# Kernel optimization log

Measured on AMD Instinct MI355X. Metric: run time of the kernel, lower is better.

Reference implementation:

```python
import jax, jax.numpy as jnp
import numpy as np

B, IN_UNIT, C, U, OUT = 256, 8, 1152, 10, 16  # batch, input_unit, input_channels, num_unit, unit_size
NUM_ROUTES = 4


def squash(s, axis):
    # norm_sqr/(1+norm_sqr) * s/||s||, matching the torch squash (no eps, as in source)
    n2 = jnp.sum(s * s, axis=axis, keepdims=True)
    return n2 / (1.0 + n2) * (s / jnp.sqrt(n2))


def setup_inputs() -> dict:
    key = jax.random.key(0)
    k1, k2 = jax.random.split(key)
    x = jax.random.normal(k1, (B, IN_UNIT, C), dtype=jnp.float32)
    W = jax.random.normal(k2, (C, U, OUT, IN_UNIT), dtype=jnp.float32)  # torch weights squeezed of leading 1
    return {"x": x, "W": W}


def reference(x, W):
    # x: [B, in_unit, C] -> [B, C, in_unit]
    xt = jnp.transpose(x, (0, 2, 1))
    # predict_vectors u_hat[b,c,u,:] = W[c,u] @ x[b,c]  -> [B, C, U, OUT]
    u_hat = jnp.einsum('bci,cuoi->bcuo', xt, W)
    b = jnp.zeros((C, U), dtype=x.dtype)  # routing logits (torch: [1,C,U,1] zeros)
    v = None
    for _ in range(NUM_ROUTES):
        c = jax.nn.softmax(b, axis=1)                      # softmax over num_unit (dim=2 in torch layout)
        s = jnp.einsum('cu,bcuo->buo', c, u_hat)           # weighted sum over input capsules -> [B,U,OUT]
        v = squash(s, axis=2)                              # squash over unit_size dim
        agreement = jnp.einsum('bcuo,buo->bcu', u_hat, v)  # u_hat^T v, -> [B,C,U]
        b = b + jnp.mean(agreement, axis=0)                # mean over batch, as in source
    return v[..., None]  # [B, U, OUT, 1] matching vec_out.squeeze(1)
```

## Files before the change

kernel.cpp:

```cpp
#include <hip/hip_runtime.h>
#include <cstdint>
#include <cstddef>

typedef _Float16 half_t;
typedef __attribute__((ext_vector_type(8))) _Float16 f16x8;
typedef __attribute__((ext_vector_type(4))) _Float16 f16x4;
typedef __attribute__((ext_vector_type(4))) float f32x4;
typedef unsigned int uint_t;

#define OFF_WH   0
#define OFF_XHF  2949120
#define OFF_XKH  7667712
#define OFF_VHF  12386304
#define OFF_AG   12468224
#define WS_NEED  12606464

__device__ __forceinline__ void gload16(const void* g, void* l) {
  __builtin_amdgcn_global_load_lds(
      (const __attribute__((address_space(1))) unsigned int*)g,
      (__attribute__((address_space(3))) unsigned int*)l, 16, 0, 0);
}

__global__ void k_setup(const float* __restrict__ x, const float* __restrict__ W,
                        half_t* __restrict__ wh, half_t* __restrict__ xhf,
                        half_t* __restrict__ xkh) {
  int bid = blockIdx.x, tid = threadIdx.x;
  if (bid < 720) {
    int gid = bid * 256 + tid;
    const float4 a0 = *(const float4*)(W + (size_t)gid * 8);
    const float4 a1 = *(const float4*)(W + (size_t)gid * 8 + 4);
    f16x8 o;
    o[0] = (half_t)a0.x; o[1] = (half_t)a0.y; o[2] = (half_t)a0.z; o[3] = (half_t)a0.w;
    o[4] = (half_t)a1.x; o[5] = (half_t)a1.y; o[6] = (half_t)a1.z; o[7] = (half_t)a1.w;
    *(f16x8*)(wh + (size_t)gid * 8) = o;
  } else if (bid < 976) {
    int b = bid - 720;
    __shared__ float lds_f[9216];
    const float4* xr = (const float4*)(x + (size_t)b * 9216);
    for (int t = tid; t < 2304; t += 256) {
      float4 v = xr[t];
      lds_f[t * 4 + 0] = v.x; lds_f[t * 4 + 1] = v.y;
      lds_f[t * 4 + 2] = v.z; lds_f[t * 4 + 3] = v.w;
    }
    __syncthreads();
    for (int t = tid; t < 1152; t += 256) {
      f16x8 o;
#pragma unroll
      for (int i = 0; i < 8; ++i) o[i] = (half_t)lds_f[i * 1152 + t];
      *(f16x8*)(xhf + (size_t)b * 9216 + t * 8) = o;
    }
  } else {
    int tb = bid - 976;
    int kt = tb % 288, bt = tb / 288;
    int c0 = kt * 4, b0 = bt * 32;
    __shared__ float lt[32][36];
    int bl = tid >> 3, ch = tid & 7;
    float4 v = *(const float4*)(x + (size_t)(b0 + bl) * 9216 + ch * 1152 + c0);
    lt[bl][0 * 8 + ch] = v.x;
    lt[bl][1 * 8 + ch] = v.y;
    lt[bl][2 * 8 + ch] = v.z;
    lt[bl][3 * 8 + ch] = v.w;
    __syncthreads();
    int kl = tid >> 3, bg = tid & 7;
    f16x4 h;
    h[0] = (half_t)lt[bg * 4 + 0][kl];
    h[1] = (half_t)lt[bg * 4 + 1][kl];
    h[2] = (half_t)lt[bg * 4 + 2][kl];
    h[3] = (half_t)lt[bg * 4 + 3][kl];
    *(f16x4*)(xkh + (size_t)(kt * 32 + kl) * 256 + b0 + bg * 4) = h;
  }
}

__global__ __launch_bounds__(1024) void k_g1sq(const half_t* __restrict__ xhf,
                                               const half_t* __restrict__ wh,
                                               const float* __restrict__ ag,
                                               half_t* __restrict__ vhfT,
                                               float* __restrict__ out, int it) {
  int mb = blockIdx.x, nt = blockIdx.y;
  int tid = threadIdx.x;
  int wv = tid >> 6, l = tid & 63, lm = l & 15, lgp = l >> 4;
  __shared__ __align__(16) half_t cwf[1152];
  __shared__ __align__(16) half_t stage[16][3][2][512];
  __shared__ __align__(16) float red[16][64][4];

  for (int c = tid; c < 1152; c += 1024) {
    float lv[10] = {0.f, 0.f, 0.f, 0.f, 0.f, 0.f, 0.f, 0.f, 0.f, 0.f};
    for (int t = 0; t < it; ++t)
#pragma unroll
      for (int u = 0; u < 10; ++u) lv[u] += ag[(size_t)(t * 10 + u) * 1152 + c];
    float mx = lv[0];
#pragma unroll
    for (int u = 1; u < 10; ++u) mx = fmaxf(mx, lv[u]);
    float ssum = 0.f, sel = 0.f;
#pragma unroll
    for (int u = 0; u < 10; ++u) {
      float e = __expf((lv[u] - mx) * (1.0f / 256.0f));
      ssum += e;
      if (u == nt) sel = e;
    }
    cwf[c] = (half_t)(sel / ssum);
  }
  __syncthreads();

  const half_t* xbase = xhf + (size_t)(mb * 16 + (l >> 2)) * 9216 + (l & 3) * 8;
  const half_t* wbase = wh + ((size_t)(lgp * 10 + nt) * 16 + lm) * 8;
  int kt0 = wv * 18;
  int cbase = kt0 * 4 + lgp;
#define ISSUE(J)                                                                   \
  do {                                                                             \
    int kt_ = kt0 + (J);                                                           \
    gload16(xbase + (size_t)kt_ * 32, &stage[wv][(J) % 3][0][0]);                  \
    gload16(wbase + (size_t)kt_ * 5120, &stage[wv][(J) % 3][1][0]);                \
  } while (0)

  ISSUE(0);
  ISSUE(1);
  ISSUE(2);

  f32x4 acc0 = {0.f, 0.f, 0.f, 0.f};
  f32x4 acc1 = {0.f, 0.f, 0.f, 0.f};
#pragma unroll
  for (int j = 0; j < 18; ++j) {
    const int buf = j % 3;
    if (j <= 15) {
      asm volatile("s_waitcnt vmcnt(4)" ::: "memory");
    } else if (j == 16) {
      asm volatile("s_waitcnt vmcnt(2)" ::: "memory");
    } else {
      asm volatile("s_waitcnt vmcnt(0)" ::: "memory");
    }
    __builtin_amdgcn_sched_barrier(0);
    f16x8 af = *(const f16x8*)&stage[wv][buf][0][lm * 32 + lgp * 8];
    f16x8 wf = *(const f16x8*)&stage[wv][buf][1][l * 8];
    half_t sc = cwf[cbase + j * 4];
    f16x8 bsc = wf * sc;
    if ((j & 1) == 0) acc0 = __builtin_amdgcn_mfma_f32_16x16x32_f16(af, bsc, acc0, 0, 0, 0);
    else              acc1 = __builtin_amdgcn_mfma_f32_16x16x32_f16(af, bsc, acc1, 0, 0, 0);
    __builtin_amdgcn_sched_barrier(0);
    if (j + 3 < 18) ISSUE(j + 3);
    __builtin_amdgcn_sched_barrier(0);
  }
#undef ISSUE
  acc0[0] += acc1[0]; acc0[1] += acc1[1]; acc0[2] += acc1[2]; acc0[3] += acc1[3];
  *(f32x4*)&red[wv][l][0] = acc0;
  __syncthreads();
  if (wv == 0) {
    float4 s = make_float4(0.f, 0.f, 0.f, 0.f);
#pragma unroll
    for (int w = 0; w < 16; ++w) {
      s.x += red[w][l][0]; s.y += red[w][l][1];
      s.z += red[w][l][2]; s.w += red[w][l][3];
    }
    float4 n2 = make_float4(s.x * s.x, s.y * s.y, s.z * s.z, s.w * s.w);
#pragma unroll
    for (int off = 1; off < 16; off <<= 1) {
      n2.x += __shfl_xor(n2.x, off);
      n2.y += __shfl_xor(n2.y, off);
      n2.z += __shfl_xor(n2.z, off);
      n2.w += __shfl_xor(n2.w, off);
    }
    float4 vv;
    vv.x = s.x * (n2.x / ((1.f + n2.x) * sqrtf(n2.x)));
    vv.y = s.y * (n2.y / ((1.f + n2.y) * sqrtf(n2.y)));
    vv.z = s.z * (n2.z / ((1.f + n2.z) * sqrtf(n2.z)));
    vv.w = s.w * (n2.w / ((1.f + n2.w) * sqrtf(n2.w)));
    if (it == 3) {
      float* ob = out + (size_t)(mb * 16 + lgp * 4) * 160 + nt * 16 + lm;
      ob[0 * 160] = vv.x; ob[1 * 160] = vv.y; ob[2 * 160] = vv.z; ob[3 * 160] = vv.w;
    } else {
      f16x4 h;
      h[0] = (half_t)vv.x; h[1] = (half_t)vv.y; h[2] = (half_t)vv.z; h[3] = (half_t)vv.w;
      *(f16x4*)(vhfT + (size_t)(nt * 16 + lm) * 256 + mb * 16 + lgp * 4) = h;
    }
  }
}

__global__ __launch_bounds__(256) void k_g2(const half_t* __restrict__ xkh,
                                            const half_t* __restrict__ vhfT,
                                            const float* __restrict__ W,
                                            float* __restrict__ ag, int it) {
  int cb = blockIdx.x;
  int tid = threadIdx.x;
  int wv = tid >> 6, l = tid & 63, lm = l & 15, lgp = l >> 4;
  int mt = cb * 4 + wv;
  f32x4 z = {0.f, 0.f, 0.f, 0.f};
  f32x4 acc[10];
#pragma unroll
  for (int nt = 0; nt < 10; ++nt) acc[nt] = z;

#pragma unroll
  for (int bt = 0; bt < 8; ++bt) {
    f16x8 af = *(const f16x8*)(xkh + (size_t)(mt * 16 + lm) * 256 + bt * 32 + lgp * 8);
#pragma unroll
    for (int nt = 0; nt < 10; ++nt) {
      f16x8 bfr = *(const f16x8*)(vhfT + (size_t)(nt * 16 + lm) * 256 + bt * 32 + lgp * 8);
      acc[nt] = __builtin_amdgcn_mfma_f32_16x16x32_f16(af, bfr, acc[nt], 0, 0, 0);
    }
  }
  int cc = mt * 2 + (lgp >> 1);
  int i0 = (lgp & 1) * 4;
  float* agt = ag + (size_t)it * 11520;
#pragma unroll
  for (int nt = 0; nt < 10; ++nt) {
    float4 wdv = *(const float4*)(W + ((size_t)(cc * 10 + nt) * 16 + lm) * 8 + i0);
    float q = acc[nt][0] * wdv.x + acc[nt][1] * wdv.y
            + acc[nt][2] * wdv.z + acc[nt][3] * wdv.w;
    q += __shfl_xor(q, 1);
    q += __shfl_xor(q, 2);
    q += __shfl_xor(q, 4);
    q += __shfl_xor(q, 8);
    q += __shfl_xor(q, 16);
    if (lm == 0 && (lgp & 1) == 0)
      agt[(size_t)nt * 1152 + cc] = q;
  }
}

extern "C" void kernel_launch(void* const* d_in, const int* in_sizes, int n_in,
                              void* d_out, int out_size, void* d_ws, size_t ws_size,
                              hipStream_t stream) {
  const float* x = (const float*)d_in[0];
  const float* W = (const float*)d_in[1];
  float* out = (float*)d_out;
  char* ws = (char*)d_ws;
  if (ws_size < WS_NEED) return;

  half_t* wh  = (half_t*)(ws + OFF_WH);
  half_t* xhf = (half_t*)(ws + OFF_XHF);
  half_t* xkh = (half_t*)(ws + OFF_XKH);
  half_t* vhfT= (half_t*)(ws + OFF_VHF);
  float*  ag  = (float*)(ws + OFF_AG);

  k_setup<<<dim3(3280), dim3(256), 0, stream>>>(x, W, wh, xhf, xkh);
  for (int it = 0; it < 4; ++it) {
    k_g1sq<<<dim3(16, 10), dim3(1024), 0, stream>>>(xhf, wh, ag, vhfT, out, it);
    if (it < 3)
      k_g2<<<dim3(144), dim3(256), 0, stream>>>(xkh, vhfT, W, ag, it);
  }
}
```

Baseline: 121.3 us.

## Fuse routing softmax into agreement kernel and deepen g1 load pipeline

The softmax over routing logits moves out of every k_g1sq block and into k_g2. k_g2 now accumulates the logits in place and writes fp16 coupling weights once per channel, so each of the 160 g1 blocks no longer re-reads all past agreement slices and recomputes the exponentials. The first iteration uses a constant 0.1 weight. The g1 LDS staging ring also grows from 3 to 4 buffers with matching waitcnt thresholds, for more loads in flight, at the cost of extra shared memory per block.

```diff
diff --git a/kernel.cpp b/kernel.cpp
--- a/kernel.cpp
+++ b/kernel.cpp
@@ -12,8 +12,9 @@
 #define OFF_XHF  2949120
 #define OFF_XKH  7667712
 #define OFF_VHF  12386304
-#define OFF_AG   12468224
-#define WS_NEED  12606464
+#define OFF_LG   12468224
+#define OFF_CWH  12514304
+#define WS_NEED  12537344
 
 __device__ __forceinline__ void gload16(const void* g, void* l) {
   __builtin_amdgcn_global_load_lds(
@@ -23,7 +24,7 @@
 
 __global__ void k_setup(const float* __restrict__ x, const float* __restrict__ W,
                         half_t* __restrict__ wh, half_t* __restrict__ xhf,
-                        half_t* __restrict__ xkh) {
+                        half_t* __restrict__ xkh, float* __restrict__ lg) {
   int bid = blockIdx.x, tid = threadIdx.x;
   if (bid < 720) {
     int gid = bid * 256 + tid;
@@ -49,7 +50,7 @@
       for (int i = 0; i < 8; ++i) o[i] = (half_t)lds_f[i * 1152 + t];
       *(f16x8*)(xhf + (size_t)b * 9216 + t * 8) = o;
     }
-  } else {
+  } else if (bid < 3280) {
     int tb = bid - 976;
     int kt = tb % 288, bt = tb / 288;
     int c0 = kt * 4, b0 = bt * 32;
@@ -68,37 +69,27 @@
     h[2] = (half_t)lt[bg * 4 + 2][kl];
     h[3] = (half_t)lt[bg * 4 + 3][kl];
     *(f16x4*)(xkh + (size_t)(kt * 32 + kl) * 256 + b0 + bg * 4) = h;
+  } else {
+    lg[(bid - 3280) * 256 + tid] = 0.f;
   }
 }
 
 __global__ __launch_bounds__(1024) void k_g1sq(const half_t* __restrict__ xhf,
                                                const half_t* __restrict__ wh,
-                                               const float* __restrict__ ag,
+                                               const half_t* __restrict__ cwh,
                                                half_t* __restrict__ vhfT,
                                                float* __restrict__ out, int it) {
   int mb = blockIdx.x, nt = blockIdx.y;
   int tid = threadIdx.x;
   int wv = tid >> 6, l = tid & 63, lm = l & 15, lgp = l >> 4;
   __shared__ __align__(16) half_t cwf[1152];
-  __shared__ __align__(16) half_t stage[16][3][2][512];
+  __shared__ __align__(16) half_t stage[16][4][2][512];
   __shared__ __align__(16) float red[16][64][4];
 
-  for (int c = tid; c < 1152; c += 1024) {
-    float lv[10] = {0.f, 0.f, 0.f, 0.f, 0.f, 0.f, 0.f, 0.f, 0.f, 0.f};
-    for (int t = 0; t < it; ++t)
-#pragma unroll
-      for (int u = 0; u < 10; ++u) lv[u] += ag[(size_t)(t * 10 + u) * 1152 + c];
-    float mx = lv[0];
-#pragma unroll
-    for (int u = 1; u < 10; ++u) mx = fmaxf(mx, lv[u]);
-    float ssum = 0.f, sel = 0.f;
-#pragma unroll
-    for (int u = 0; u < 10; ++u) {
-      float e = __expf((lv[u] - mx) * (1.0f / 256.0f));
-      ssum += e;
-      if (u == nt) sel = e;
-    }
-    cwf[c] = (half_t)(sel / ssum);
+  if (it == 0) {
+    for (int c = tid; c < 1152; c += 1024) cwf[c] = (half_t)0.1f;
+  } else {
+    for (int c = tid; c < 1152; c += 1024) cwf[c] = cwh[(size_t)nt * 1152 + c];
   }
   __syncthreads();
 
@@ -109,20 +100,23 @@
 #define ISSUE(J)                                                                   \
   do {                                                                             \
     int kt_ = kt0 + (J);                                                           \
-    gload16(xbase + (size_t)kt_ * 32, &stage[wv][(J) % 3][0][0]);                  \
-    gload16(wbase + (size_t)kt_ * 5120, &stage[wv][(J) % 3][1][0]);                \
+    gload16(xbase + (size_t)kt_ * 32, &stage[wv][(J) % 4][0][0]);                  \
+    gload16(wbase + (size_t)kt_ * 5120, &stage[wv][(J) % 4][1][0]);                \
   } while (0)
 
   ISSUE(0);
   ISSUE(1);
   ISSUE(2);
+  ISSUE(3);
 
   f32x4 acc0 = {0.f, 0.f, 0.f, 0.f};
   f32x4 acc1 = {0.f, 0.f, 0.f, 0.f};
 #pragma unroll
   for (int j = 0; j < 18; ++j) {
-    const int buf = j % 3;
-    if (j <= 15) {
+    const int buf = j % 4;
+    if (j <= 14) {
+      asm volatile("s_waitcnt vmcnt(6)" ::: "memory");
+    } else if (j == 15) {
       asm volatile("s_waitcnt vmcnt(4)" ::: "memory");
     } else if (j == 16) {
       asm volatile("s_waitcnt vmcnt(2)" ::: "memory");
@@ -137,7 +131,7 @@
     if ((j & 1) == 0) acc0 = __builtin_amdgcn_mfma_f32_16x16x32_f16(af, bsc, acc0, 0, 0, 0);
     else              acc1 = __builtin_amdgcn_mfma_f32_16x16x32_f16(af, bsc, acc1, 0, 0, 0);
     __builtin_amdgcn_sched_barrier(0);
-    if (j + 3 < 18) ISSUE(j + 3);
+    if (j + 4 < 18) ISSUE(j + 4);
     __builtin_amdgcn_sched_barrier(0);
   }
 #undef ISSUE
@@ -178,11 +172,13 @@
 __global__ __launch_bounds__(256) void k_g2(const half_t* __restrict__ xkh,
                                             const half_t* __restrict__ vhfT,
                                             const float* __restrict__ W,
-                                            float* __restrict__ ag, int it) {
+                                            float* __restrict__ lg,
+                                            half_t* __restrict__ cwh) {
   int cb = blockIdx.x;
   int tid = threadIdx.x;
   int wv = tid >> 6, l = tid & 63, lm = l & 15, lgp = l >> 4;
   int mt = cb * 4 + wv;
+  __shared__ float sm[8][10];
   f32x4 z = {0.f, 0.f, 0.f, 0.f};
   f32x4 acc[10];
 #pragma unroll
@@ -199,7 +195,7 @@
   }
   int cc = mt * 2 + (lgp >> 1);
   int i0 = (lgp & 1) * 4;
-  float* agt = ag + (size_t)it * 11520;
+  int cl = wv * 2 + (lgp >> 1);
 #pragma unroll
   for (int nt = 0; nt < 10; ++nt) {
     float4 wdv = *(const float4*)(W + ((size_t)(cc * 10 + nt) * 16 + lm) * 8 + i0);
@@ -210,8 +206,30 @@
     q += __shfl_xor(q, 4);
     q += __shfl_xor(q, 8);
     q += __shfl_xor(q, 16);
-    if (lm == 0 && (lgp & 1) == 0)
-      agt[(size_t)nt * 1152 + cc] = q;
+    if (lm == 0 && (lgp & 1) == 0) sm[cl][nt] = q;
+  }
+  __syncthreads();
+  if (tid < 8) {
+    int c = cb * 8 + tid;
+    float lv[10];
+    float mx = -1e30f;
+#pragma unroll
+    for (int u = 0; u < 10; ++u) {
+      float nlg = lg[(size_t)u * 1152 + c] + sm[tid][u];
+      lg[(size_t)u * 1152 + c] = nlg;
+      lv[u] = nlg;
+      mx = fmaxf(mx, nlg);
+    }
+    float ssum = 0.f;
+#pragma unroll
+    for (int u = 0; u < 10; ++u) {
+      lv[u] = __expf((lv[u] - mx) * (1.0f / 256.0f));
+      ssum += lv[u];
+    }
+    float inv = 1.f / ssum;
+#pragma unroll
+    for (int u = 0; u < 10; ++u)
+      cwh[(size_t)u * 1152 + c] = (half_t)(lv[u] * inv);
   }
 }
 
@@ -228,12 +246,13 @@
   half_t* xhf = (half_t*)(ws + OFF_XHF);
   half_t* xkh = (half_t*)(ws + OFF_XKH);
   half_t* vhfT= (half_t*)(ws + OFF_VHF);
-  float*  ag  = (float*)(ws + OFF_AG);
-
-  k_setup<<<dim3(3280), dim3(256), 0, stream>>>(x, W, wh, xhf, xkh);
+  float*  lg  = (float*)(ws + OFF_LG);
+  half_t* cwh = (half_t*)(ws + OFF_CWH);
+
+  k_setup<<<dim3(3325), dim3(256), 0, stream>>>(x, W, wh, xhf, xkh, lg);
   for (int it = 0; it < 4; ++it) {
-    k_g1sq<<<dim3(16, 10), dim3(1024), 0, stream>>>(xhf, wh, ag, vhfT, out, it);
+    k_g1sq<<<dim3(16, 10), dim3(1024), 0, stream>>>(xhf, wh, cwh, vhfT, out, it);
     if (it < 3)
-      k_g2<<<dim3(144), dim3(256), 0, stream>>>(xkh, vhfT, W, ag, it);
-  }
-}
+      k_g2<<<dim3(144), dim3(256), 0, stream>>>(xkh, vhfT, W, lg, cwh);
+  }
+}
```

After: 114.2 us. -5.8%, faster.
